# Optimization experiments

Hardware: AMD Instinct MI355X
Metric: run time of the kernel (lower is better)

The kernel has to match this reference:

```python
import jax, jax.numpy as jnp
import numpy as np

D_K = 64
D_MODEL = 1024
N_HEADS = 16


def setup_inputs() -> dict:
    key = jax.random.key(0)
    ks = jax.random.split(key, 9)
    B, S = 2, 2048
    scale = 1.0 / np.sqrt(D_MODEL)
    inp = {
        "x": jax.random.normal(ks[0], (B, S, D_MODEL), dtype=jnp.float32),
        "w_q": jax.random.normal(ks[1], (D_MODEL, N_HEADS * D_K), dtype=jnp.float32) * scale,
        "b_q": jnp.zeros((N_HEADS * D_K,), dtype=jnp.float32),
        "w_k": jax.random.normal(ks[2], (D_MODEL, N_HEADS * D_K), dtype=jnp.float32) * scale,
        "b_k": jnp.zeros((N_HEADS * D_K,), dtype=jnp.float32),
        "w_v": jax.random.normal(ks[3], (D_MODEL, N_HEADS * D_K), dtype=jnp.float32) * scale,
        "b_v": jnp.zeros((N_HEADS * D_K,), dtype=jnp.float32),
        "w_o": jax.random.normal(ks[4], (N_HEADS * D_K, D_MODEL), dtype=jnp.float32) * scale,
        "b_o": jnp.zeros((D_MODEL,), dtype=jnp.float32),
    }
    return inp


def reference(x, w_q, b_q, w_k, b_k, w_v, b_v, w_o, b_o):
    B, S, _ = x.shape
    H, Dk = N_HEADS, D_K

    def split_heads(m):  # [B,S,H*Dk] -> [B,H,S,Dk]
        return m.reshape(B, S, H, Dk).transpose(0, 2, 1, 3)

    Q = split_heads(x @ w_q + b_q)
    K = split_heads(x @ w_k + b_k)
    V = split_heads(x @ w_v + b_v)

    scores = jnp.einsum("bhsd,bhtd->bhst", Q, K) / jnp.sqrt(jnp.float32(Dk))
    probs = jax.nn.softmax(scores, axis=-1)
    attn = jnp.einsum("bhst,bhtd->bhsd", probs, V)  # [B,H,S,Dk]
    attn = attn.transpose(0, 2, 1, 3).reshape(B, S, H * Dk)
    return attn @ w_o + b_o
```

## Files before the change

### kernel.cpp

```cpp
#include <hip/hip_runtime.h>
#include <math.h>

#define D_MODELc 1024
#define N_HEADSc 16
#define D_Kc     64
#define B_SZc    2
#define S_LENc   2048
#define NTOKc    (B_SZc * S_LENc)

using half8  = __attribute__((ext_vector_type(8))) _Float16;
using half4  = __attribute__((ext_vector_type(4))) _Float16;
using fp16x2 = __attribute__((ext_vector_type(2))) __fp16;
using float4v = __attribute__((ext_vector_type(4))) float;

__global__ __launch_bounds__(256) void cvt_all(
    const float* __restrict__ x,
    const float* __restrict__ W0, const float* __restrict__ W1,
    const float* __restrict__ W2, const float* __restrict__ W3,
    _Float16* __restrict__ wout, _Float16* __restrict__ xout)
{
    __shared__ float T[32][33];
    const int z = blockIdx.z;
    const int t = threadIdx.x;

    if (z == 4) {
        const int bid = blockIdx.y * 32 + blockIdx.x;
        #pragma unroll
        for (int c = 0; c < 2; ++c) {
            const int i = bid * 512 + c * 256 + t;
            float4v a = ((const float4v*)x)[2 * i];
            float4v b = ((const float4v*)x)[2 * i + 1];
            half8 h;
            h[0] = (_Float16)a[0]; h[1] = (_Float16)a[1];
            h[2] = (_Float16)a[2]; h[3] = (_Float16)a[3];
            h[4] = (_Float16)b[0]; h[5] = (_Float16)b[1];
            h[6] = (_Float16)b[2]; h[7] = (_Float16)b[3];
            ((half8*)xout)[i] = h;
        }
        return;
    }

    const float* W = (z == 0) ? W0 : (z == 1) ? W1 : (z == 2) ? W2 : W3;
    _Float16* O = wout + (size_t)z * 1024 * 1024;

    const int k0 = blockIdx.x * 32;
    const int n0 = blockIdx.y * 32;
    {
        const int r = t >> 3, c4 = (t & 7) * 4;
        float4v v = *(const float4v*)(W + (size_t)(k0 + r) * 1024 + n0 + c4);
        T[r][c4 + 0] = v[0]; T[r][c4 + 1] = v[1];
        T[r][c4 + 2] = v[2]; T[r][c4 + 3] = v[3];
    }
    __syncthreads();
    {
        const int rn = t >> 3, ck4 = (t & 7) * 4;
        half4 h;
        h[0] = (_Float16)T[ck4 + 0][rn];
        h[1] = (_Float16)T[ck4 + 1][rn];
        h[2] = (_Float16)T[ck4 + 2][rn];
        h[3] = (_Float16)T[ck4 + 3][rn];
        *(half4*)(O + (size_t)(n0 + rn) * 1024 + k0 + ck4) = h;
    }
}

__global__ __launch_bounds__(256) void gemm_qkv(
    const _Float16* __restrict__ A, const _Float16* __restrict__ BtAll,
    const float* __restrict__ bias0, const float* __restrict__ bias1,
    const float* __restrict__ bias2, _Float16* __restrict__ Cout)
{
    __shared__ _Float16 Als[2][128 * 32];
    __shared__ _Float16 Bls[2][128 * 32];

    constexpr int K = 1024;
    const int tid = threadIdx.x;
    const int m0  = blockIdx.x * 128;
    const int n0  = blockIdx.y * 128;
    const int z   = blockIdx.z;

    const _Float16* Bt  = BtAll + (size_t)z * 1024 * 1024;
    const float* bias   = (z == 0) ? bias0 : (z == 1) ? bias1 : bias2;
    const float qscale  = (z == 0) ? 0.18033688011112042f : 1.0f;

    const int wave = tid >> 6, lane = tid & 63;
    const int wr = wave >> 1, wc = wave & 1;
    const int quad = lane >> 4, l16 = lane & 15;

    float4v acc[4][4];
    #pragma unroll
    for (int i = 0; i < 4; ++i)
        #pragma unroll
        for (int j = 0; j < 4; ++j)
            acc[i][j] = (float4v){0.f, 0.f, 0.f, 0.f};

    for (int k0 = 0; k0 < K; k0 += 64) {
        #pragma unroll
        for (int c = 0; c < 2; ++c) {
            const int i   = c * 256 + tid;
            const int row = i >> 2, kc = i & 3;
            #pragma unroll
            for (int h = 0; h < 2; ++h) {
                __builtin_amdgcn_global_load_lds(
                    (const __attribute__((address_space(1))) void*)
                        (A + (size_t)(m0 + row) * K + k0 + h * 32 + kc * 8),
                    (__attribute__((address_space(3))) void*)(Als[h] + i * 8),
                    16, 0, 0);
                __builtin_amdgcn_global_load_lds(
                    (const __attribute__((address_space(1))) void*)
                        (Bt + (size_t)(n0 + row) * K + k0 + h * 32 + kc * 8),
                    (__attribute__((address_space(3))) void*)(Bls[h] + i * 8),
                    16, 0, 0);
            }
        }
        __syncthreads();

        half8 af[4][2], bf[4][2];
        #pragma unroll
        for (int i = 0; i < 4; ++i) {
            const int r = (wr * 64 + i * 16 + l16) * 32 + quad * 8;
            af[i][0] = *(const half8*)(Als[0] + r);
            af[i][1] = *(const half8*)(Als[1] + r);
        }
        #pragma unroll
        for (int j = 0; j < 4; ++j) {
            const int r = (wc * 64 + j * 16 + l16) * 32 + quad * 8;
            bf[j][0] = *(const half8*)(Bls[0] + r);
            bf[j][1] = *(const half8*)(Bls[1] + r);
        }
        #pragma unroll
        for (int i = 0; i < 4; ++i)
            #pragma unroll
            for (int j = 0; j < 4; ++j) {
                acc[i][j] = __builtin_amdgcn_mfma_f32_16x16x32_f16(
                    af[i][0], bf[j][0], acc[i][j], 0, 0, 0);
                acc[i][j] = __builtin_amdgcn_mfma_f32_16x16x32_f16(
                    af[i][1], bf[j][1], acc[i][j], 0, 0, 0);
            }
        __syncthreads();
    }

    if (z != 2) {
        _Float16* C = Cout + (size_t)z * NTOKc * D_MODELc;
        #pragma unroll
        for (int i = 0; i < 4; ++i) {
            const int rbase = m0 + wr * 64 + i * 16 + quad * 4;
            #pragma unroll
            for (int j = 0; j < 4; ++j) {
                const int col = n0 + wc * 64 + j * 16 + l16;
                const float bv = bias[col];
                #pragma unroll
                for (int r = 0; r < 4; ++r)
                    C[(size_t)(rbase + r) * 1024 + col] =
                        (_Float16)((acc[i][j][r] + bv) * qscale);
            }
        }
    } else {
        #pragma unroll
        for (int i = 0; i < 4; ++i) {
            const int rbase = m0 + wr * 64 + i * 16 + quad * 4;
            const int b = rbase >> 11, s0 = rbase & 2047;
            #pragma unroll
            for (int j = 0; j < 4; ++j) {
                const int col = n0 + wc * 64 + j * 16 + l16;
                const float bv = bias[col];
                const int h = col >> 6, d = col & 63;
                half4 hv;
                #pragma unroll
                for (int r = 0; r < 4; ++r)
                    hv[r] = (_Float16)(acc[i][j][r] + bv);
                _Float16* C = Cout + (size_t)2 * NTOKc * D_MODELc;
                *(half4*)(C + (((size_t)(b * N_HEADSc + h)) * D_Kc + d) *
                          S_LENc + s0) = hv;
            }
        }
    }
}

__global__ __launch_bounds__(256) void gemm_out(
    const _Float16* __restrict__ A, const _Float16* __restrict__ Bt,
    const float* __restrict__ bias, float* __restrict__ C)
{
    __shared__ _Float16 Als[2][64 * 32];
    __shared__ _Float16 Bls[2][128 * 32];

    constexpr int K = 1024;
    const int tid = threadIdx.x;
    const int m0  = blockIdx.x * 64;
    const int n0  = blockIdx.y * 128;

    const int wave = tid >> 6, lane = tid & 63;
    const int wr = wave >> 1, wc = wave & 1;
    const int quad = lane >> 4, l16 = lane & 15;

    float4v acc[2][4];
    #pragma unroll
    for (int i = 0; i < 2; ++i)
        #pragma unroll
        for (int j = 0; j < 4; ++j)
            acc[i][j] = (float4v){0.f, 0.f, 0.f, 0.f};

    for (int k0 = 0; k0 < K; k0 += 64) {
        {
            const int row = tid >> 2, kc = tid & 3;
            #pragma unroll
            for (int h = 0; h < 2; ++h)
                __builtin_amdgcn_global_load_lds(
                    (const __attribute__((address_space(1))) void*)
                        (A + (size_t)(m0 + row) * K + k0 + h * 32 + kc * 8),
                    (__attribute__((address_space(3))) void*)(Als[h] + tid * 8),
                    16, 0, 0);
        }
        #pragma unroll
        for (int c = 0; c < 2; ++c) {
            const int i = c * 256 + tid;
            const int row = i >> 2, kc = i & 3;
            #pragma unroll
            for (int h = 0; h < 2; ++h)
                __builtin_amdgcn_global_load_lds(
                    (const __attribute__((address_space(1))) void*)
                        (Bt + (size_t)(n0 + row) * K + k0 + h * 32 + kc * 8),
                    (__attribute__((address_space(3))) void*)(Bls[h] + i * 8),
                    16, 0, 0);
        }
        __syncthreads();

        half8 af[2][2], bf[4][2];
        #pragma unroll
        for (int i = 0; i < 2; ++i) {
            const int r = (wr * 32 + i * 16 + l16) * 32 + quad * 8;
            af[i][0] = *(const half8*)(Als[0] + r);
            af[i][1] = *(const half8*)(Als[1] + r);
        }
        #pragma unroll
        for (int j = 0; j < 4; ++j) {
            const int r = (wc * 64 + j * 16 + l16) * 32 + quad * 8;
            bf[j][0] = *(const half8*)(Bls[0] + r);
            bf[j][1] = *(const half8*)(Bls[1] + r);
        }
        #pragma unroll
        for (int i = 0; i < 2; ++i)
            #pragma unroll
            for (int j = 0; j < 4; ++j) {
                acc[i][j] = __builtin_amdgcn_mfma_f32_16x16x32_f16(
                    af[i][0], bf[j][0], acc[i][j], 0, 0, 0);
                acc[i][j] = __builtin_amdgcn_mfma_f32_16x16x32_f16(
                    af[i][1], bf[j][1], acc[i][j], 0, 0, 0);
            }
        __syncthreads();
    }

    #pragma unroll
    for (int i = 0; i < 2; ++i) {
        const int rbase = m0 + wr * 32 + i * 16 + quad * 4;
        #pragma unroll
        for (int j = 0; j < 4; ++j) {
            const int col = n0 + wc * 64 + j * 16 + l16;
            const float bv = bias[col];
            #pragma unroll
            for (int r = 0; r < 4; ++r)
                C[(size_t)(rbase + r) * 1024 + col] = acc[i][j][r] + bv;
        }
    }
}

__global__ __launch_bounds__(256) void attn_mfma(
    const _Float16* __restrict__ Qt, const _Float16* __restrict__ Kt,
    const _Float16* __restrict__ Vtg, _Float16* __restrict__ Ab)
{
    __shared__ _Float16 Ks[2][64 * 64];
    __shared__ _Float16 Vt[64 * 64];
    __shared__ _Float16 Ps[64 * 64];

    const int tid  = threadIdx.x;
    const int wv   = tid >> 6;
    const int lane = tid & 63;
    const int quad = lane >> 4;
    const int l16  = lane & 15;
    const int rotl = (l16 & 7) << 3;
    const int cA   = (quad * 8 + rotl) & 63;
    const int cB   = (quad * 8 + 32 + rotl) & 63;

    const int q0 = blockIdx.x * 64;
    const int bh = blockIdx.y;
    const int b  = bh >> 4, h = bh & 15;

    const _Float16* Qsl = Qt + (size_t)b * S_LENc * D_MODELc + h * 64;
    const _Float16* Ksl = Kt + (size_t)b * S_LENc * D_MODELc + h * 64;
    const _Float16* Vsl = Vtg + (size_t)bh * S_LENc * D_Kc;

    const int sR = tid >> 3;
    const int sC = (((tid & 7) - ((tid >> 3) & 7)) & 7) << 3;
    const _Float16* gK = Ksl + (size_t)sR * D_MODELc + sC;
    const _Float16* gV = Vsl + (size_t)sR * S_LENc + sC;

#define STAGE_K(BUF, T0)                                                     \
    {                                                                        \
        _Pragma("unroll")                                                    \
        for (int c = 0; c < 2; ++c)                                          \
            __builtin_amdgcn_global_load_lds(                                \
                (const __attribute__((address_space(1))) void*)              \
                    (gK + (size_t)((T0) + c * 32) * D_MODELc),               \
                (__attribute__((address_space(3))) void*)                    \
                    (Ks[BUF] + tid * 8 + c * 2048),                          \
                16, 0, 0);                                                   \
    }
#define STAGE_V(T0)                                                          \
    {                                                                        \
        _Pragma("unroll")                                                    \
        for (int c = 0; c < 2; ++c)                                          \
            __builtin_amdgcn_global_load_lds(                                \
                (const __attribute__((address_space(1))) void*)              \
                    (gV + (T0) + c * 32 * S_LENc),                           \
                (__attribute__((address_space(3))) void*)                    \
                    (Vt + tid * 8 + c * 2048),                               \
                16, 0, 0);                                                   \
    }

    half8 aq[2];
    {
        const _Float16* qp = Qsl + (size_t)(q0 + wv * 16 + l16) * D_MODELc;
        aq[0] = *(const half8*)(qp + quad * 8);
        aq[1] = *(const half8*)(qp + 32 + quad * 8);
    }

    half8 vones;
    #pragma unroll
    for (int j = 0; j < 8; ++j) vones[j] = (_Float16)1.0f;

    float4v O[4];
    #pragma unroll
    for (int nt = 0; nt < 4; ++nt)
        O[nt] = (float4v){0.f, 0.f, 0.f, 0.f};
    float4v Lacc = (float4v){0.f, 0.f, 0.f, 0.f};

    STAGE_K(0, 0);
    STAGE_V(0);

    int cur = 0;
    for (int t0 = 0; t0 < S_LENc; t0 += 64) {
        __syncthreads();
        if (t0 != 0)
            STAGE_V(t0);

        const _Float16* KsC = Ks[cur];
        half8 kf[4][2];
        #pragma unroll
        for (int nt = 0; nt < 4; ++nt) {
            const int base = (nt * 16 + l16) * 64;
            kf[nt][0] = *(const half8*)(KsC + base + cA);
            kf[nt][1] = *(const half8*)(KsC + base + cB);
        }

        float4v st[4];
        __builtin_amdgcn_s_setprio(1);
        #pragma unroll
        for (int nt = 0; nt < 4; ++nt) {
            st[nt] = __builtin_amdgcn_mfma_f32_16x16x32_f16(
                kf[nt][0], aq[0], (float4v){0.f, 0.f, 0.f, 0.f}, 0, 0, 0);
            st[nt] = __builtin_amdgcn_mfma_f32_16x16x32_f16(
                kf[nt][1], aq[1], st[nt], 0, 0, 0);
        }
        __builtin_amdgcn_s_setprio(0);

        const int rowP = (wv * 16 + l16) * 64;
        #pragma unroll
        for (int nt = 0; nt < 4; ++nt) {
            const float p0 = __builtin_amdgcn_exp2f(fminf(st[nt][0], 15.5f));
            const float p1 = __builtin_amdgcn_exp2f(fminf(st[nt][1], 15.5f));
            const float p2 = __builtin_amdgcn_exp2f(fminf(st[nt][2], 15.5f));
            const float p3 = __builtin_amdgcn_exp2f(fminf(st[nt][3], 15.5f));
            union { fp16x2 h2[2]; half4 h4; } u;
            u.h2[0] = __builtin_amdgcn_cvt_pkrtz(p0, p1);
            u.h2[1] = __builtin_amdgcn_cvt_pkrtz(p2, p3);
            *(half4*)(Ps + rowP + ((nt * 16 + quad * 4 + rotl) & 63)) = u.h4;
        }

        __syncthreads();
        if (t0 + 64 < S_LENc)
            STAGE_K(cur ^ 1, t0 + 64);

        half8 bvv[4][2];
        #pragma unroll
        for (int nt = 0; nt < 4; ++nt) {
            const int base = (nt * 16 + l16) * 64;
            bvv[nt][0] = *(const half8*)(Vt + base + cA);
            bvv[nt][1] = *(const half8*)(Vt + base + cB);
        }
        half8 ap0 = *(const half8*)(Ps + rowP + cA);
        half8 ap1 = *(const half8*)(Ps + rowP + cB);
        __builtin_amdgcn_s_setprio(1);
        #pragma unroll
        for (int nt = 0; nt < 4; ++nt) {
            O[nt] = __builtin_amdgcn_mfma_f32_16x16x32_f16(
                ap0, bvv[nt][0], O[nt], 0, 0, 0);
            O[nt] = __builtin_amdgcn_mfma_f32_16x16x32_f16(
                ap1, bvv[nt][1], O[nt], 0, 0, 0);
        }
        Lacc = __builtin_amdgcn_mfma_f32_16x16x32_f16(ap0, vones, Lacc, 0, 0, 0);
        Lacc = __builtin_amdgcn_mfma_f32_16x16x32_f16(ap1, vones, Lacc, 0, 0, 0);
        __builtin_amdgcn_s_setprio(0);
        cur ^= 1;
    }
#undef STAGE_K
#undef STAGE_V

    _Float16* Asl = Ab + (size_t)b * S_LENc * D_MODELc + h * 64;
    #pragma unroll
    for (int r = 0; r < 4; ++r) {
        const float inv = 1.0f / Lacc[r];
        const int q = q0 + wv * 16 + quad * 4 + r;
        _Float16* dst = Asl + (size_t)q * D_MODELc;
        #pragma unroll
        for (int nt = 0; nt < 4; ++nt)
            dst[nt * 16 + l16] = (_Float16)(O[nt][r] * inv);
    }
}

extern "C" void kernel_launch(void* const* d_in, const int* in_sizes, int n_in,
                              void* d_out, int out_size, void* d_ws, size_t ws_size,
                              hipStream_t stream)
{
    const float* x  = (const float*)d_in[0];
    const float* wq = (const float*)d_in[1];
    const float* bq = (const float*)d_in[2];
    const float* wk = (const float*)d_in[3];
    const float* bk = (const float*)d_in[4];
    const float* wv = (const float*)d_in[5];
    const float* bv = (const float*)d_in[6];
    const float* wo = (const float*)d_in[7];
    const float* bo = (const float*)d_in[8];
    float* out = (float*)d_out;

    const size_t M1 = 1024 * 1024;
    const size_t M4 = 4 * M1;
    _Float16* xh = (_Float16*)d_ws;
    _Float16* wh = xh + M4;
    _Float16* Qh = wh + M4;
    _Float16* Ah = xh;

    cvt_all<<<dim3(32, 32, 5), dim3(256), 0, stream>>>(
        x, wq, wk, wv, wo, wh, xh);
    gemm_qkv<<<dim3(NTOKc / 128, D_MODELc / 128, 3), dim3(256), 0, stream>>>(
        xh, wh, bq, bk, bv, Qh);
    attn_mfma<<<dim3(S_LENc / 64, B_SZc * N_HEADSc), dim3(256), 0, stream>>>(
        Qh, Qh + M4, Qh + 2 * M4, Ah);
    gemm_out<<<dim3(NTOKc / 64, D_MODELc / 128), dim3(256), 0, stream>>>(
        Ah, wh + 3 * M1, bo, out);
}
```

Before: 204.3 us.

## Repartition attention warps over key/dim columns instead of query rows

Each wave now owns a 16-key slice for QK^T and a 16-dim slice of V for PV, covering all 64 queries, instead of owning 16 query rows across all keys and dims. This cuts per-wave LDS reads of K and V fragments to one fragment pair and holds all four Q fragments in registers. In exchange it reads four P fragments per wave, adds a data-dependent branch for the row-sum MFMA, and shares row sums through LDS with an extra barrier. The output store pattern also changes.

```diff
diff --git a/kernel.cpp b/kernel.cpp
--- a/kernel.cpp
+++ b/kernel.cpp
@@ -269,6 +269,7 @@
     __shared__ _Float16 Ks[2][64 * 64];
     __shared__ _Float16 Vt[64 * 64];
     __shared__ _Float16 Ps[64 * 64];
+    __shared__ float Lsh[64];
 
     const int tid  = threadIdx.x;
     const int wv   = tid >> 6;
@@ -315,11 +316,12 @@
                 16, 0, 0);                                                   \
     }
 
-    half8 aq[2];
-    {
-        const _Float16* qp = Qsl + (size_t)(q0 + wv * 16 + l16) * D_MODELc;
-        aq[0] = *(const half8*)(qp + quad * 8);
-        aq[1] = *(const half8*)(qp + 32 + quad * 8);
+    half8 aq[4][2];
+    #pragma unroll
+    for (int qf = 0; qf < 4; ++qf) {
+        const _Float16* qp = Qsl + (size_t)(q0 + qf * 16 + l16) * D_MODELc;
+        aq[qf][0] = *(const half8*)(qp + quad * 8);
+        aq[qf][1] = *(const half8*)(qp + 32 + quad * 8);
     }
 
     half8 vones;
@@ -328,8 +330,8 @@
 
     float4v O[4];
     #pragma unroll
-    for (int nt = 0; nt < 4; ++nt)
-        O[nt] = (float4v){0.f, 0.f, 0.f, 0.f};
+    for (int qf = 0; qf < 4; ++qf)
+        O[qf] = (float4v){0.f, 0.f, 0.f, 0.f};
     float4v Lacc = (float4v){0.f, 0.f, 0.f, 0.f};
 
     STAGE_K(0, 0);
@@ -342,76 +344,81 @@
             STAGE_V(t0);
 
         const _Float16* KsC = Ks[cur];
-        half8 kf[4][2];
-        #pragma unroll
-        for (int nt = 0; nt < 4; ++nt) {
-            const int base = (nt * 16 + l16) * 64;
-            kf[nt][0] = *(const half8*)(KsC + base + cA);
-            kf[nt][1] = *(const half8*)(KsC + base + cB);
-        }
-
+        const int kbase = (wv * 16 + l16) * 64;
+        half8 kf0 = *(const half8*)(KsC + kbase + cA);
+        half8 kf1 = *(const half8*)(KsC + kbase + cB);
+
+        __builtin_amdgcn_s_setprio(1);
         float4v st[4];
-        __builtin_amdgcn_s_setprio(1);
-        #pragma unroll
-        for (int nt = 0; nt < 4; ++nt) {
-            st[nt] = __builtin_amdgcn_mfma_f32_16x16x32_f16(
-                kf[nt][0], aq[0], (float4v){0.f, 0.f, 0.f, 0.f}, 0, 0, 0);
-            st[nt] = __builtin_amdgcn_mfma_f32_16x16x32_f16(
-                kf[nt][1], aq[1], st[nt], 0, 0, 0);
+        #pragma unroll
+        for (int qf = 0; qf < 4; ++qf) {
+            st[qf] = __builtin_amdgcn_mfma_f32_16x16x32_f16(
+                kf0, aq[qf][0], (float4v){0.f, 0.f, 0.f, 0.f}, 0, 0, 0);
+            st[qf] = __builtin_amdgcn_mfma_f32_16x16x32_f16(
+                kf1, aq[qf][1], st[qf], 0, 0, 0);
         }
         __builtin_amdgcn_s_setprio(0);
 
-        const int rowP = (wv * 16 + l16) * 64;
-        #pragma unroll
-        for (int nt = 0; nt < 4; ++nt) {
-            const float p0 = __builtin_amdgcn_exp2f(fminf(st[nt][0], 15.5f));
-            const float p1 = __builtin_amdgcn_exp2f(fminf(st[nt][1], 15.5f));
-            const float p2 = __builtin_amdgcn_exp2f(fminf(st[nt][2], 15.5f));
-            const float p3 = __builtin_amdgcn_exp2f(fminf(st[nt][3], 15.5f));
+        #pragma unroll
+        for (int qf = 0; qf < 4; ++qf) {
+            const float p0 = __builtin_amdgcn_exp2f(fminf(st[qf][0], 15.5f));
+            const float p1 = __builtin_amdgcn_exp2f(fminf(st[qf][1], 15.5f));
+            const float p2 = __builtin_amdgcn_exp2f(fminf(st[qf][2], 15.5f));
+            const float p3 = __builtin_amdgcn_exp2f(fminf(st[qf][3], 15.5f));
             union { fp16x2 h2[2]; half4 h4; } u;
             u.h2[0] = __builtin_amdgcn_cvt_pkrtz(p0, p1);
             u.h2[1] = __builtin_amdgcn_cvt_pkrtz(p2, p3);
-            *(half4*)(Ps + rowP + ((nt * 16 + quad * 4 + rotl) & 63)) = u.h4;
+            *(half4*)(Ps + (qf * 16 + l16) * 64 +
+                      ((wv * 16 + quad * 4 + rotl) & 63)) = u.h4;
         }
 
         __syncthreads();
         if (t0 + 64 < S_LENc)
             STAGE_K(cur ^ 1, t0 + 64);
 
-        half8 bvv[4][2];
-        #pragma unroll
-        for (int nt = 0; nt < 4; ++nt) {
-            const int base = (nt * 16 + l16) * 64;
-            bvv[nt][0] = *(const half8*)(Vt + base + cA);
-            bvv[nt][1] = *(const half8*)(Vt + base + cB);
-        }
-        half8 ap0 = *(const half8*)(Ps + rowP + cA);
-        half8 ap1 = *(const half8*)(Ps + rowP + cB);
+        const int vbase = (wv * 16 + l16) * 64;
+        half8 bv0 = *(const half8*)(Vt + vbase + cA);
+        half8 bv1 = *(const half8*)(Vt + vbase + cB);
+
         __builtin_amdgcn_s_setprio(1);
         #pragma unroll
-        for (int nt = 0; nt < 4; ++nt) {
-            O[nt] = __builtin_amdgcn_mfma_f32_16x16x32_f16(
-                ap0, bvv[nt][0], O[nt], 0, 0, 0);
-            O[nt] = __builtin_amdgcn_mfma_f32_16x16x32_f16(
-                ap1, bvv[nt][1], O[nt], 0, 0, 0);
-        }
-        Lacc = __builtin_amdgcn_mfma_f32_16x16x32_f16(ap0, vones, Lacc, 0, 0, 0);
-        Lacc = __builtin_amdgcn_mfma_f32_16x16x32_f16(ap1, vones, Lacc, 0, 0, 0);
+        for (int qf = 0; qf < 4; ++qf) {
+            const int rowP = (qf * 16 + l16) * 64;
+            half8 ap0 = *(const half8*)(Ps + rowP + cA);
+            half8 ap1 = *(const half8*)(Ps + rowP + cB);
+            O[qf] = __builtin_amdgcn_mfma_f32_16x16x32_f16(
+                ap0, bv0, O[qf], 0, 0, 0);
+            O[qf] = __builtin_amdgcn_mfma_f32_16x16x32_f16(
+                ap1, bv1, O[qf], 0, 0, 0);
+            if (qf == wv) {
+                Lacc = __builtin_amdgcn_mfma_f32_16x16x32_f16(
+                    ap0, vones, Lacc, 0, 0, 0);
+                Lacc = __builtin_amdgcn_mfma_f32_16x16x32_f16(
+                    ap1, vones, Lacc, 0, 0, 0);
+            }
+        }
         __builtin_amdgcn_s_setprio(0);
         cur ^= 1;
     }
 #undef STAGE_K
 #undef STAGE_V
 
+    if (l16 == 0) {
+        #pragma unroll
+        for (int r = 0; r < 4; ++r)
+            Lsh[wv * 16 + quad * 4 + r] = Lacc[r];
+    }
+    __syncthreads();
     _Float16* Asl = Ab + (size_t)b * S_LENc * D_MODELc + h * 64;
     #pragma unroll
-    for (int r = 0; r < 4; ++r) {
-        const float inv = 1.0f / Lacc[r];
-        const int q = q0 + wv * 16 + quad * 4 + r;
-        _Float16* dst = Asl + (size_t)q * D_MODELc;
-        #pragma unroll
-        for (int nt = 0; nt < 4; ++nt)
-            dst[nt * 16 + l16] = (_Float16)(O[nt][r] * inv);
+    for (int qf = 0; qf < 4; ++qf) {
+        #pragma unroll
+        for (int r = 0; r < 4; ++r) {
+            const int qr = qf * 16 + quad * 4 + r;
+            const float inv = 1.0f / Lsh[qr];
+            Asl[(size_t)(q0 + qr) * D_MODELc + wv * 16 + l16] =
+                (_Float16)(O[qf][r] * inv);
+        }
     }
 }
 
```

After: 206.9 us. Within noise of the previous version (+1.3%).

## Double-buffer V tiles, drop mid-loop barrier, remap blocks for XCD locality

Applied to the files above, without the earlier changes.

The attention kernel now double-buffers the V tile in shared memory. Both the next K and V tiles are issued at the top of each iteration, which removes the second __syncthreads per loop. This relies on each wave reading only its own rows of the Ps scratch tile. Both the QKV GEMM and the attention kernel also remap flat block IDs so that blocks sharing operands land on the same XCD, to improve L2 reuse. The extra V buffer raises LDS use per block, which may lower occupancy.

```diff
diff --git a/kernel.cpp b/kernel.cpp
--- a/kernel.cpp
+++ b/kernel.cpp
@@ -73,9 +73,13 @@
 
     constexpr int K = 1024;
     const int tid = threadIdx.x;
-    const int m0  = blockIdx.x * 128;
-    const int n0  = blockIdx.y * 128;
-    const int z   = blockIdx.z;
+
+    const int flat = blockIdx.x + 32 * blockIdx.y + 256 * blockIdx.z;
+    const int xcd  = flat & 7;
+    const int slot = flat >> 3;
+    const int m0   = ((xcd & 3) * 8 + (slot & 7)) * 128;
+    const int n0   = ((xcd >> 2) * 4 + ((slot >> 3) & 3)) * 128;
+    const int z    = slot >> 5;
 
     const _Float16* Bt  = BtAll + (size_t)z * 1024 * 1024;
     const float* bias   = (z == 0) ? bias0 : (z == 1) ? bias1 : bias2;
@@ -267,7 +271,7 @@
     const _Float16* __restrict__ Vtg, _Float16* __restrict__ Ab)
 {
     __shared__ _Float16 Ks[2][64 * 64];
-    __shared__ _Float16 Vt[64 * 64];
+    __shared__ _Float16 Vt[2][64 * 64];
     __shared__ _Float16 Ps[64 * 64];
 
     const int tid  = threadIdx.x;
@@ -279,8 +283,10 @@
     const int cA   = (quad * 8 + rotl) & 63;
     const int cB   = (quad * 8 + 32 + rotl) & 63;
 
-    const int q0 = blockIdx.x * 64;
-    const int bh = blockIdx.y;
+    const int flat = blockIdx.x + 32 * blockIdx.y;
+    const int slot = flat >> 3;
+    const int bh   = (flat & 7) + 8 * (slot >> 5);
+    const int q0   = (slot & 31) * 64;
     const int b  = bh >> 4, h = bh & 15;
 
     const _Float16* Qsl = Qt + (size_t)b * S_LENc * D_MODELc + h * 64;
@@ -303,7 +309,7 @@
                     (Ks[BUF] + tid * 8 + c * 2048),                          \
                 16, 0, 0);                                                   \
     }
-#define STAGE_V(T0)                                                          \
+#define STAGE_V(BUF, T0)                                                     \
     {                                                                        \
         _Pragma("unroll")                                                    \
         for (int c = 0; c < 2; ++c)                                          \
@@ -311,7 +317,7 @@
                 (const __attribute__((address_space(1))) void*)              \
                     (gV + (T0) + c * 32 * S_LENc),                           \
                 (__attribute__((address_space(3))) void*)                    \
-                    (Vt + tid * 8 + c * 2048),                               \
+                    (Vt[BUF] + tid * 8 + c * 2048),                          \
                 16, 0, 0);                                                   \
     }
 
@@ -333,13 +339,15 @@
     float4v Lacc = (float4v){0.f, 0.f, 0.f, 0.f};
 
     STAGE_K(0, 0);
-    STAGE_V(0);
+    STAGE_V(0, 0);
 
     int cur = 0;
     for (int t0 = 0; t0 < S_LENc; t0 += 64) {
         __syncthreads();
-        if (t0 != 0)
-            STAGE_V(t0);
+        if (t0 + 64 < S_LENc) {
+            STAGE_K(cur ^ 1, t0 + 64);
+            STAGE_V(cur ^ 1, t0 + 64);
+        }
 
         const _Float16* KsC = Ks[cur];
         half8 kf[4][2];
@@ -374,16 +382,13 @@
             *(half4*)(Ps + rowP + ((nt * 16 + quad * 4 + rotl) & 63)) = u.h4;
         }
 
-        __syncthreads();
-        if (t0 + 64 < S_LENc)
-            STAGE_K(cur ^ 1, t0 + 64);
-
+        const _Float16* VtC = Vt[cur];
         half8 bvv[4][2];
         #pragma unroll
         for (int nt = 0; nt < 4; ++nt) {
             const int base = (nt * 16 + l16) * 64;
-            bvv[nt][0] = *(const half8*)(Vt + base + cA);
-            bvv[nt][1] = *(const half8*)(Vt + base + cB);
+            bvv[nt][0] = *(const half8*)(VtC + base + cA);
+            bvv[nt][1] = *(const half8*)(VtC + base + cB);
         }
         half8 ap0 = *(const half8*)(Ps + rowP + cA);
         half8 ap1 = *(const half8*)(Ps + rowP + cB);
```

After: 205.6 us. Within noise of the previous version (+0.6%).
